# Kernel optimization log

Hardware: AMD Instinct MI355X
Metric: run time of the kernel (lower is better)

## Reference

```python
import jax, jax.numpy as jnp
import numpy as np

BIG = 1e10  # sentinel for masked min/max (squared distances are << BIG)


def _boundary_mask(img, num_classes):
    """Union over classes v>0 of pixels adjacent (4-neighborhood) to a class change.
    Matches extract_boundaries: final (boundaries > 0) is the union of per-class masks."""
    b = jnp.zeros(img.shape, dtype=bool)
    for v in range(1, num_classes):
        m = img == v
        dv = m[:-1, :] != m[1:, :]   # vertical neighbor differs
        dh = m[:, :-1] != m[:, 1:]   # horizontal neighbor differs
        b = b | jnp.pad(dv, ((0, 1), (0, 0))) | jnp.pad(dv, ((1, 0), (0, 0)))
        b = b | jnp.pad(dh, ((0, 0), (0, 1))) | jnp.pad(dh, ((0, 0), (1, 0)))
    return b


def _pairwise_sqdist(H, W):
    ii, jj = jnp.meshgrid(jnp.arange(H), jnp.arange(W), indexing='ij')
    coords = jnp.stack([ii.ravel(), jj.ravel()], axis=1).astype(jnp.float32)  # [N,2]
    sq = jnp.sum(coords * coords, axis=1)
    d2 = sq[:, None] + sq[None, :] - 2.0 * (coords @ coords.T)  # [N,N]
    return jnp.maximum(d2, 0.0)


def _hausdorff(m1, m2, d2):
    # directed(A->B) on SQUARED distances (sqrt is monotone, applied once at the end)
    min_to2 = jnp.min(jnp.where(m2[None, :], d2, BIG), axis=1)   # [N] nearest pt in set2
    fwd = jnp.max(jnp.where(m1, min_to2, -BIG))
    min_to1 = jnp.min(jnp.where(m1[None, :], d2, BIG), axis=1)
    bwd = jnp.max(jnp.where(m2, min_to1, -BIG))
    return jnp.sqrt(jnp.maximum(jnp.maximum(fwd, bwd), 0.0))


def setup_inputs() -> dict:
    key = jax.random.key(0)
    k1, k2 = jax.random.split(key)
    B, C, H, W = 4, 4, 96, 96
    output = jax.random.normal(k1, (B, C, H, W), dtype=jnp.float32)
    target = jax.random.randint(k2, (B, H, W), 0, C, dtype=jnp.int32)
    return {"output": output, "target": target}


def reference(output, target):
    B, C, H, W = output.shape
    pred = jnp.argmax(output, axis=1)  # [B,H,W]
    mask_pred = jax.vmap(lambda im: _boundary_mask(im, C))(pred).reshape(B, -1)
    mask_tgt = jax.vmap(lambda im: _boundary_mask(im, C))(target).reshape(B, -1)
    d2 = _pairwise_sqdist(H, W)  # shared [N,N] grid distances
    dists = jax.lax.map(lambda mm: _hausdorff(mm[0], mm[1], d2), (mask_pred, mask_tgt))
    return dists.mean()
```

## Files before the change

kernel.cpp:

```cpp
#include <hip/hip_runtime.h>
#include <math.h>

#define BB 4
#define CC 4
#define HH 96
#define WW 96
#define NN (HH * WW)
#define WPR (WW / 4)
#define NW (NN / 4)
#define BIGF 1e10f
#define OROWS (HH / 8)

__global__ __launch_bounds__(1024) void k_fused(const float* __restrict__ out,
                                                const int* __restrict__ tgt,
                                                float* __restrict__ partial) {
    __shared__ __align__(16) unsigned char smem[64512];
    unsigned char* predL  = smem;
    unsigned char* tgtL   = smem + 9216;
    float* gq             = (float*)smem;
    unsigned char* maskE  = smem + 36864;
    unsigned char* maskO  = smem + 46080;
    unsigned int* colbits = (unsigned int*)(smem + 55296);
    float* red            = (float*)(smem + 57216);

    const int blk = blockIdx.x;
    const int oct = blk & 7;
    const int e = (blk >> 3) & 1;
    const int b = blk >> 4;
    const int tid = threadIdx.x;

    const float* obase = out + (size_t)b * CC * NN;
    const int* tbase = tgt + b * NN;
    {
        const int w0 = tid, w1 = tid + 1024, w2 = tid + 2048;
        const bool has2 = (tid < NW - 2048);
        const int p0 = w0 * 4, p1 = w1 * 4, p2 = has2 ? w2 * 4 : 0;

        float4 a0 = *(const float4*)(obase + p0);
        float4 a1 = *(const float4*)(obase + NN + p0);
        float4 a2 = *(const float4*)(obase + 2 * NN + p0);
        float4 a3 = *(const float4*)(obase + 3 * NN + p0);
        float4 b0 = *(const float4*)(obase + p1);
        float4 b1 = *(const float4*)(obase + NN + p1);
        float4 b2 = *(const float4*)(obase + 2 * NN + p1);
        float4 b3 = *(const float4*)(obase + 3 * NN + p1);
        float4 c0 = *(const float4*)(obase + p2);
        float4 c1 = *(const float4*)(obase + NN + p2);
        float4 c2 = *(const float4*)(obase + 2 * NN + p2);
        float4 c3 = *(const float4*)(obase + 3 * NN + p2);
        int4 t0 = *(const int4*)(tbase + p0);
        int4 t1 = *(const int4*)(tbase + p1);
        int4 t2 = *(const int4*)(tbase + p2);

        #define AMAX4(r0, r1, r2, r3, sh, pk) {            \
            float bv = (r0); unsigned int bc = 0;          \
            if ((r1) > bv) { bv = (r1); bc = 1; }          \
            if ((r2) > bv) { bv = (r2); bc = 2; }          \
            if ((r3) > bv) { bv = (r3); bc = 3; }          \
            pk |= bc << (sh); }
        unsigned int pk0 = 0, pk1 = 0, pk2 = 0;
        AMAX4(a0.x, a1.x, a2.x, a3.x, 0,  pk0) AMAX4(a0.y, a1.y, a2.y, a3.y, 8,  pk0)
        AMAX4(a0.z, a1.z, a2.z, a3.z, 16, pk0) AMAX4(a0.w, a1.w, a2.w, a3.w, 24, pk0)
        AMAX4(b0.x, b1.x, b2.x, b3.x, 0,  pk1) AMAX4(b0.y, b1.y, b2.y, b3.y, 8,  pk1)
        AMAX4(b0.z, b1.z, b2.z, b3.z, 16, pk1) AMAX4(b0.w, b1.w, b2.w, b3.w, 24, pk1)
        AMAX4(c0.x, c1.x, c2.x, c3.x, 0,  pk2) AMAX4(c0.y, c1.y, c2.y, c3.y, 8,  pk2)
        AMAX4(c0.z, c1.z, c2.z, c3.z, 16, pk2) AMAX4(c0.w, c1.w, c2.w, c3.w, 24, pk2)
        #undef AMAX4

        ((unsigned int*)predL)[w0] = pk0;
        ((unsigned int*)predL)[w1] = pk1;
        ((unsigned int*)tgtL)[w0] =
            (t0.x & 0xFF) | ((t0.y & 0xFF) << 8) | ((t0.z & 0xFF) << 16) | ((t0.w & 0xFF) << 24);
        ((unsigned int*)tgtL)[w1] =
            (t1.x & 0xFF) | ((t1.y & 0xFF) << 8) | ((t1.z & 0xFF) << 16) | ((t1.w & 0xFF) << 24);
        if (has2) {
            ((unsigned int*)predL)[w2] = pk2;
            ((unsigned int*)tgtL)[w2] =
                (t2.x & 0xFF) | ((t2.y & 0xFF) << 8) | ((t2.z & 0xFF) << 16) | ((t2.w & 0xFF) << 24);
        }
    }
    __syncthreads();

    const unsigned int* pw = (const unsigned int*)predL;
    const unsigned int* tw = (const unsigned int*)tgtL;
    for (int w = tid; w < NW; w += 1024) {
        int i = w / WPR;
        int jw = w - i * WPR;
        unsigned int mP, mT;
        #pragma unroll
        for (int s = 0; s < 2; ++s) {
            const unsigned int* src = s ? tw : pw;
            unsigned int c = src[w];
            unsigned int diff = 0;
            if (i > 0)      diff |= c ^ src[w - WPR];
            if (i < HH - 1) diff |= c ^ src[w + WPR];
            unsigned int l = (c << 8) | (jw > 0 ? (src[w - 1] >> 24) : (c & 0xFFu));
            diff |= c ^ l;
            unsigned int r = (c >> 8) | (jw < WPR - 1 ? (src[w + 1] << 24) : (c & 0xFF000000u));
            diff |= c ^ r;
            unsigned int y = (((diff & 0x7F7F7F7Fu) + 0x7F7F7F7Fu) | diff) & 0x80808080u;
            unsigned int m01 = (y >> 7);
            if (s) mT = m01; else mP = m01;
        }
        ((unsigned int*)maskE)[w] = e ? mT : mP;
        ((unsigned int*)maskO)[w] = e ? mP : mT;
    }
    __syncthreads();

    if (tid < 96 * 3) {
        int j = tid / 3, w = tid - j * 3;
        const unsigned char* colp = &maskE[w * 32 * WW + j];
        unsigned int bits = 0;
        #pragma unroll
        for (int r = 0; r < 32; ++r) bits |= ((unsigned int)colp[r * WW]) << r;
        colbits[j * 5 + w] = bits;
    }
    __syncthreads();

    const int pix0 = oct * OROWS * WW;
    for (int p4 = tid; p4 < OROWS * WW; p4 += 1024) {
        int p = pix0 + p4;
        int i = p / WW;
        int j = p - i * WW;
        unsigned int w0 = colbits[j * 5 + 0];
        unsigned int w1 = colbits[j * 5 + 1];
        unsigned int hi = colbits[j * 5 + 2];
        unsigned long long lo = (unsigned long long)w0 | ((unsigned long long)w1 << 32);
        int up = 1 << 20, dn = 1 << 20;
        if (i < 64) {
            unsigned long long mu = lo & (~0ull >> (63 - i));
            if (mu) up = i - (63 - __clzll(mu));
            unsigned long long md = lo >> i;
            if (md) dn = __ffsll(md) - 1;
            else if (hi) dn = (64 - i) + (__ffs(hi) - 1);
        } else {
            int ih = i - 64;
            unsigned int mu = hi & (0xFFFFFFFFu >> (31 - ih));
            if (mu) up = ih - (31 - __clz(mu));
            else if (lo) up = i - (63 - __clzll(lo));
            unsigned int md = hi >> ih;
            if (md) dn = __ffs(md) - 1;
        }
        int d = (up < dn) ? up : dn;
        gq[p] = (d < HH) ? (float)(d * d) : BIGF;
    }
    __syncthreads();

    float m = -BIGF;
    for (int p4 = tid; p4 < OROWS * WW; p4 += 1024) {
        int p = pix0 + p4;
        if (!maskO[p]) continue;
        int i = p / WW;
        int j = p - i * WW;
        const float* grow = &gq[i * WW];
        float best = grow[j];
        for (int o = 1; o < WW; ++o) {
            float o2 = (float)(o * o);
            if (o2 >= best) break;
            int jl = j - o, jr = j + o;
            if (jl >= 0)  best = fminf(best, grow[jl] + o2);
            if (jr < WW)  best = fminf(best, grow[jr] + o2);
        }
        m = fmaxf(m, best);
    }
    #pragma unroll
    for (int off = 32; off > 0; off >>= 1) m = fmaxf(m, __shfl_down(m, off));
    const int wid = tid >> 6, lid = tid & 63;
    if (lid == 0) red[wid] = m;
    __syncthreads();
    if (tid == 0) {
        float mm = red[0];
        #pragma unroll
        for (int w = 1; w < 16; ++w) mm = fmaxf(mm, red[w]);
        partial[blk] = mm;
    }
}

__global__ void k_fin(const float* __restrict__ partial, float* __restrict__ outv) {
    if (threadIdx.x == 0) {
        float s = 0.0f;
        #pragma unroll
        for (int b = 0; b < BB; ++b) {
            float bwd = -BIGF, fwd = -BIGF;
            #pragma unroll
            for (int oo = 0; oo < 8; ++oo) {
                bwd = fmaxf(bwd, partial[b * 16 + oo]);
                fwd = fmaxf(fwd, partial[b * 16 + 8 + oo]);
            }
            s += sqrtf(fmaxf(fmaxf(fwd, bwd), 0.0f));
        }
        outv[0] = s * 0.25f;
    }
}

extern "C" void kernel_launch(void* const* d_in, const int* in_sizes, int n_in,
                              void* d_out, int out_size, void* d_ws, size_t ws_size,
                              hipStream_t stream) {
    const float* output = (const float*)d_in[0];
    const int* target   = (const int*)d_in[1];
    float* outv         = (float*)d_out;
    float* partial      = (float*)d_ws;

    k_fused<<<64, 1024, 0, stream>>>(output, target, partial);
    k_fin<<<1, 64, 0, stream>>>(partial, outv);
}
```

Before: 61.98 us.

## Pack pred/target into one LDS word and build column bitmasks with atomics

```diff
diff --git a/kernel.cpp b/kernel.cpp
--- a/kernel.cpp
+++ b/kernel.cpp
@@ -14,9 +14,8 @@
 __global__ __launch_bounds__(1024) void k_fused(const float* __restrict__ out,
                                                 const int* __restrict__ tgt,
                                                 float* __restrict__ partial) {
-    __shared__ __align__(16) unsigned char smem[64512];
-    unsigned char* predL  = smem;
-    unsigned char* tgtL   = smem + 9216;
+    __shared__ __align__(16) unsigned char smem[57344];
+    unsigned int* comb    = (unsigned int*)smem;
     float* gq             = (float*)smem;
     unsigned char* maskE  = smem + 36864;
     unsigned char* maskO  = smem + 46080;
@@ -29,91 +28,98 @@
     const int b = blk >> 4;
     const int tid = threadIdx.x;
 
-    const float* obase = out + (size_t)b * CC * NN;
+    if (tid < 96 * 5) colbits[tid] = 0;
+
+    const float* o0 = out + (size_t)b * CC * NN;
+    const float* o1 = o0 + NN;
+    const float* o2 = o0 + 2 * NN;
+    const float* o3 = o0 + 3 * NN;
     const int* tbase = tgt + b * NN;
     {
         const int w0 = tid, w1 = tid + 1024, w2 = tid + 2048;
         const bool has2 = (tid < NW - 2048);
-        const int p0 = w0 * 4, p1 = w1 * 4, p2 = has2 ? w2 * 4 : 0;
-
-        float4 a0 = *(const float4*)(obase + p0);
-        float4 a1 = *(const float4*)(obase + NN + p0);
-        float4 a2 = *(const float4*)(obase + 2 * NN + p0);
-        float4 a3 = *(const float4*)(obase + 3 * NN + p0);
-        float4 b0 = *(const float4*)(obase + p1);
-        float4 b1 = *(const float4*)(obase + NN + p1);
-        float4 b2 = *(const float4*)(obase + 2 * NN + p1);
-        float4 b3 = *(const float4*)(obase + 3 * NN + p1);
-        float4 c0 = *(const float4*)(obase + p2);
-        float4 c1 = *(const float4*)(obase + NN + p2);
-        float4 c2 = *(const float4*)(obase + 2 * NN + p2);
-        float4 c3 = *(const float4*)(obase + 3 * NN + p2);
+        const int p0 = w0 * 4, p1 = w1 * 4, p2 = w2 * 4;
+
+        float4 a0 = *(const float4*)(o0 + p0);
+        float4 a1 = *(const float4*)(o1 + p0);
+        float4 a2 = *(const float4*)(o2 + p0);
+        float4 a3 = *(const float4*)(o3 + p0);
+        float4 b0 = *(const float4*)(o0 + p1);
+        float4 b1 = *(const float4*)(o1 + p1);
+        float4 b2 = *(const float4*)(o2 + p1);
+        float4 b3 = *(const float4*)(o3 + p1);
         int4 t0 = *(const int4*)(tbase + p0);
         int4 t1 = *(const int4*)(tbase + p1);
-        int4 t2 = *(const int4*)(tbase + p2);
-
-        #define AMAX4(r0, r1, r2, r3, sh, pk) {            \
-            float bv = (r0); unsigned int bc = 0;          \
-            if ((r1) > bv) { bv = (r1); bc = 1; }          \
-            if ((r2) > bv) { bv = (r2); bc = 2; }          \
-            if ((r3) > bv) { bv = (r3); bc = 3; }          \
-            pk |= bc << (sh); }
-        unsigned int pk0 = 0, pk1 = 0, pk2 = 0;
+        float4 c0, c1, c2, c3;
+        int4 t2;
+        if (has2) {
+            c0 = *(const float4*)(o0 + p2);
+            c1 = *(const float4*)(o1 + p2);
+            c2 = *(const float4*)(o2 + p2);
+            c3 = *(const float4*)(o3 + p2);
+            t2 = *(const int4*)(tbase + p2);
+        }
+
+        #define AMAX4(v0, v1, v2, v3, sh, pk) {                          \
+            bool c01 = (v1) > (v0); float lo_ = c01 ? (v1) : (v0);       \
+            bool c23 = (v3) > (v2); float hi_ = c23 ? (v3) : (v2);       \
+            unsigned int id = (hi_ > lo_) ? (2u | (unsigned int)c23)     \
+                                          : (unsigned int)c01;           \
+            pk |= id << (sh); }
+        unsigned int pk0 = 0, pk1 = 0;
         AMAX4(a0.x, a1.x, a2.x, a3.x, 0,  pk0) AMAX4(a0.y, a1.y, a2.y, a3.y, 8,  pk0)
         AMAX4(a0.z, a1.z, a2.z, a3.z, 16, pk0) AMAX4(a0.w, a1.w, a2.w, a3.w, 24, pk0)
         AMAX4(b0.x, b1.x, b2.x, b3.x, 0,  pk1) AMAX4(b0.y, b1.y, b2.y, b3.y, 8,  pk1)
         AMAX4(b0.z, b1.z, b2.z, b3.z, 16, pk1) AMAX4(b0.w, b1.w, b2.w, b3.w, 24, pk1)
-        AMAX4(c0.x, c1.x, c2.x, c3.x, 0,  pk2) AMAX4(c0.y, c1.y, c2.y, c3.y, 8,  pk2)
-        AMAX4(c0.z, c1.z, c2.z, c3.z, 16, pk2) AMAX4(c0.w, c1.w, c2.w, c3.w, 24, pk2)
+
+        unsigned int tw0 = (t0.x & 3) | ((t0.y & 3) << 8) | ((t0.z & 3) << 16) | ((t0.w & 3) << 24);
+        unsigned int tw1 = (t1.x & 3) | ((t1.y & 3) << 8) | ((t1.z & 3) << 16) | ((t1.w & 3) << 24);
+        comb[w0] = pk0 | (tw0 << 4);
+        comb[w1] = pk1 | (tw1 << 4);
+        if (has2) {
+            unsigned int pk2 = 0;
+            AMAX4(c0.x, c1.x, c2.x, c3.x, 0,  pk2) AMAX4(c0.y, c1.y, c2.y, c3.y, 8,  pk2)
+            AMAX4(c0.z, c1.z, c2.z, c3.z, 16, pk2) AMAX4(c0.w, c1.w, c2.w, c3.w, 24, pk2)
+            unsigned int tw2 = (t2.x & 3) | ((t2.y & 3) << 8) | ((t2.z & 3) << 16) | ((t2.w & 3) << 24);
+            comb[w2] = pk2 | (tw2 << 4);
+        }
         #undef AMAX4
-
-        ((unsigned int*)predL)[w0] = pk0;
-        ((unsigned int*)predL)[w1] = pk1;
-        ((unsigned int*)tgtL)[w0] =
-            (t0.x & 0xFF) | ((t0.y & 0xFF) << 8) | ((t0.z & 0xFF) << 16) | ((t0.w & 0xFF) << 24);
-        ((unsigned int*)tgtL)[w1] =
-            (t1.x & 0xFF) | ((t1.y & 0xFF) << 8) | ((t1.z & 0xFF) << 16) | ((t1.w & 0xFF) << 24);
-        if (has2) {
-            ((unsigned int*)predL)[w2] = pk2;
-            ((unsigned int*)tgtL)[w2] =
-                (t2.x & 0xFF) | ((t2.y & 0xFF) << 8) | ((t2.z & 0xFF) << 16) | ((t2.w & 0xFF) << 24);
-        }
-    }
-    __syncthreads();
-
-    const unsigned int* pw = (const unsigned int*)predL;
-    const unsigned int* tw = (const unsigned int*)tgtL;
-    for (int w = tid; w < NW; w += 1024) {
-        int i = w / WPR;
-        int jw = w - i * WPR;
-        unsigned int mP, mT;
-        #pragma unroll
-        for (int s = 0; s < 2; ++s) {
-            const unsigned int* src = s ? tw : pw;
-            unsigned int c = src[w];
+    }
+    __syncthreads();
+
+    {
+        const unsigned int* iw = comb;
+        const int kst = tid & 3;
+        auto PROC = [&](int w) {
+            int i = w / WPR;
+            int jw = w - i * WPR;
+            unsigned int c = iw[w];
             unsigned int diff = 0;
-            if (i > 0)      diff |= c ^ src[w - WPR];
-            if (i < HH - 1) diff |= c ^ src[w + WPR];
-            unsigned int l = (c << 8) | (jw > 0 ? (src[w - 1] >> 24) : (c & 0xFFu));
+            if (i > 0)      diff |= c ^ iw[w - WPR];
+            if (i < HH - 1) diff |= c ^ iw[w + WPR];
+            unsigned int l = (c << 8) | (jw > 0 ? (iw[w - 1] >> 24) : (c & 0xFFu));
             diff |= c ^ l;
-            unsigned int r = (c >> 8) | (jw < WPR - 1 ? (src[w + 1] << 24) : (c & 0xFF000000u));
+            unsigned int r = (c >> 8) | (jw < WPR - 1 ? (iw[w + 1] << 24) : (c & 0xFF000000u));
             diff |= c ^ r;
-            unsigned int y = (((diff & 0x7F7F7F7Fu) + 0x7F7F7F7Fu) | diff) & 0x80808080u;
-            unsigned int m01 = (y >> 7);
-            if (s) mT = m01; else mP = m01;
-        }
-        ((unsigned int*)maskE)[w] = e ? mT : mP;
-        ((unsigned int*)maskO)[w] = e ? mP : mT;
-    }
-    __syncthreads();
-
-    if (tid < 96 * 3) {
-        int j = tid / 3, w = tid - j * 3;
-        const unsigned char* colp = &maskE[w * 32 * WW + j];
-        unsigned int bits = 0;
-        #pragma unroll
-        for (int r = 0; r < 32; ++r) bits |= ((unsigned int)colp[r * WW]) << r;
-        colbits[j * 5 + w] = bits;
+            unsigned int dL = diff & 0x0F0F0F0Fu;
+            unsigned int dH = (diff >> 4) & 0x0F0F0F0Fu;
+            unsigned int mP = ((dL + 0x0F0F0F0Fu) >> 4) & 0x01010101u;
+            unsigned int mT = ((dH + 0x0F0F0F0Fu) >> 4) & 0x01010101u;
+            unsigned int mE = e ? mT : mP;
+            ((unsigned int*)maskE)[w] = mE;
+            ((unsigned int*)maskO)[w] = e ? mP : mT;
+            int widx = i >> 5;
+            unsigned int bit = 1u << (i & 31);
+            #pragma unroll
+            for (int kk = 0; kk < 4; ++kk) {
+                int k = (kk + kst) & 3;
+                if ((mE >> (8 * k)) & 1u)
+                    atomicOr(&colbits[(jw * 4 + k) * 5 + widx], bit);
+            }
+        };
+        PROC(tid);
+        PROC(tid + 1024);
+        if (tid < NW - 2048) PROC(tid + 2048);
     }
     __syncthreads();
 
@@ -177,20 +183,15 @@
 }
 
 __global__ void k_fin(const float* __restrict__ partial, float* __restrict__ outv) {
-    if (threadIdx.x == 0) {
-        float s = 0.0f;
-        #pragma unroll
-        for (int b = 0; b < BB; ++b) {
-            float bwd = -BIGF, fwd = -BIGF;
-            #pragma unroll
-            for (int oo = 0; oo < 8; ++oo) {
-                bwd = fmaxf(bwd, partial[b * 16 + oo]);
-                fwd = fmaxf(fwd, partial[b * 16 + 8 + oo]);
-            }
-            s += sqrtf(fmaxf(fmaxf(fwd, bwd), 0.0f));
-        }
-        outv[0] = s * 0.25f;
-    }
+    const int t = threadIdx.x;
+    float m = partial[t];
+    m = fmaxf(m, __shfl_xor(m, 1));
+    m = fmaxf(m, __shfl_xor(m, 2));
+    m = fmaxf(m, __shfl_xor(m, 4));
+    m = fmaxf(m, __shfl_xor(m, 8));
+    float s = sqrtf(fmaxf(m, 0.0f));
+    float s0 = __shfl(s, 0), s1 = __shfl(s, 16), s2 = __shfl(s, 32), s3 = __shfl(s, 48);
+    if (t == 0) outv[0] = (s0 + s1 + s2 + s3) * 0.25f;
 }
 
 extern "C" void kernel_launch(void* const* d_in, const int* in_sizes, int n_in,
```

Result: faster. 59.66 us (-3.7%).
